# Kernel optimization log

Measured on AMD Instinct MI355X. Metric: run time of the kernel, lower is better.

The kernel has to match this reference:

```python
import jax, jax.numpy as jnp
import numpy as np
import math

B, C, H, W = 512, 64, 8, 8
E, NH, MEM = 64, 8, 8          # embed_dim, num_heads, mem_n
HD = E // NH                   # head_dim
THD = H * W * HD               # tot_head_dim = 512
AMB = 5.0                      # attn_mask_b
LN_EPS = 1e-5


def conv2d(x, w, b):
    y = jax.lax.conv_general_dilated(x, w, (1, 1), 'SAME',
                                     dimension_numbers=('NCHW', 'OIHW', 'NCHW'))
    return y + b[None, :, None, None]


def setup_inputs() -> dict:
    key = jax.random.key(0)
    ks = jax.random.split(key, 14)
    r = lambda k, s, sc=1.0: jax.random.normal(k, s, dtype=jnp.float32) * sc
    return {
        'input': r(ks[0], (B, C, H, W)),
        'h_cur': r(ks[1], (B, E, H, W)),
        'c_cur': r(ks[2], (B, E, H, W)),
        'concat_k': r(ks[3], (B, MEM, NH, THD)),
        'concat_v': r(ks[4], (B, MEM, NH, THD)),
        'attn_mask': jax.random.randint(ks[5], (B * NH, 1, MEM), 0, 2).astype(bool),
        'conv_w': r(ks[6], (5 * E, C + E, 3, 3), 0.05),
        'conv_b': jnp.zeros((5 * E,), jnp.float32),
        'proj_w': r(ks[7], (3 * E, C, 3, 3), 0.05),
        'proj_b': jnp.zeros((3 * E,), jnp.float32),
        'out_w': r(ks[8], (E, E, 3, 3), 0.05),
        'out_b': jnp.zeros((E,), jnp.float32),
        'ln_w': jnp.ones((E, H, W), jnp.float32),
        'ln_b': jnp.zeros((E, H, W), jnp.float32),
        'pos_w': r(ks[9], (MEM, H * W * E), 0.02),
        'pos_b': jax.random.uniform(ks[10], (MEM, NH), jnp.float32, -0.1, 0.1),
    }


def _cell(input, h_cur, c_cur, concat_k, concat_v, attn_mask,
          conv_w, conv_b, proj_w, proj_b, out_w, out_b, ln_w, ln_b, pos_w, pos_b):
    # ConvLSTM gates
    combined = jnp.concatenate([input, h_cur], axis=1)          # [B, C+E, H, W]
    cc = conv2d(combined, conv_w, conv_b)                       # [B, 5E, H, W]
    cc_i, cc_f, cc_o, cc_g, cc_a = jnp.split(cc, 5, axis=1)
    i = jax.nn.sigmoid(cc_i)
    f = jax.nn.sigmoid(cc_f)
    o = jax.nn.sigmoid(cc_o)
    g = jnp.tanh(cc_g)
    a = jax.nn.sigmoid(cc_a)
    c_next = f * c_cur + i * g

    # attention over growing memory
    kqv = conv2d(input, proj_w, proj_b)                         # [B, 3E, H, W]
    k, q, v = jnp.split(kqv, 3, axis=1)
    # [B, E, H, W] -> [B*NH, 1, THD] (contiguous split of E into NH heads)
    resh = lambda x: x.reshape(B * NH, 1, THD)
    k, q, v = resh(k), resh(q), resh(v)
    q_scaled = q / math.sqrt(THD)

    # prior memory: [B, MEM, NH, THD] -> [B*NH, MEM-1, THD]
    def mem_resh(m):
        return jnp.transpose(m[:, 1:], (1, 0, 2, 3)).reshape(MEM - 1, B * NH, THD).transpose(1, 0, 2)
    k_full = jnp.concatenate([mem_resh(concat_k), k], axis=1)   # [B*NH, MEM, THD]
    v_full = jnp.concatenate([mem_resh(concat_v), v], axis=1)

    # learned positional key offsets / score biases
    pos_w_e = jnp.broadcast_to(pos_w[:, None, :], (MEM, B, H * W * E)) \
                 .reshape(MEM, B * NH, THD).transpose(1, 0, 2)  # [B*NH, MEM, THD]
    pos_b_e = jnp.broadcast_to(pos_b[:, None, :], (MEM, B, NH)) \
                 .reshape(MEM, B * NH).T                        # [B*NH, MEM]
    k_full = k_full + pos_w_e

    # additive mask: -inf where masked, last slot forced to +attn_mask_b
    mask = jnp.where(attn_mask, -jnp.inf, 0.0).astype(q.dtype)  # [B*NH, 1, MEM]
    mask = mask.at[:, :, -1].set(AMB)

    scores = mask + jnp.einsum('bqd,bkd->bqk', q_scaled, k_full) + pos_b_e[:, None, :]
    w = jax.nn.softmax(scores, axis=-1)                         # [B*NH, 1, MEM]
    attn = jnp.einsum('bqk,bkd->bqd', w, v_full)                # [B*NH, 1, THD]
    attn = attn.reshape(B, E, H, W)

    out = conv2d(attn, out_w, out_b) + input[:, :E]
    # LayerNorm over (E, H, W)
    mu = jnp.mean(out, axis=(1, 2, 3), keepdims=True)
    var = jnp.mean((out - mu) ** 2, axis=(1, 2, 3), keepdims=True)
    out = (out - mu) / jnp.sqrt(var + LN_EPS) * ln_w[None] + ln_b[None]

    c_next = c_next + a * jnp.tanh(out)
    h_next = o * jnp.tanh(c_next)

    ret = lambda m: m.transpose(1, 0, 2).reshape(MEM, B, NH, THD).transpose(1, 0, 2, 3)
    return h_next, c_next, ret(k_full), ret(v_full)


def reference(input, h_cur, c_cur, concat_k, concat_v, attn_mask,
              conv_w, conv_b, proj_w, proj_b, out_w, out_b, ln_w, ln_b, pos_w, pos_b):
    return _cell(input, h_cur, c_cur, concat_k, concat_v, attn_mask,
                 conv_w, conv_b, proj_w, proj_b, out_w, out_b, ln_w, ln_b, pos_w, pos_b)
```

## Files before the change

kernel.cpp:

```cpp
#include <hip/hip_runtime.h>

typedef short short8 __attribute__((ext_vector_type(8)));
typedef __bf16 bf16x8 __attribute__((ext_vector_type(8)));
typedef float f32x4 __attribute__((ext_vector_type(4)));
typedef short s16x4 __attribute__((ext_vector_type(4)));
typedef unsigned u32x4 __attribute__((ext_vector_type(4)));

__device__ __forceinline__ short f2bf(float f) {
  unsigned u = __builtin_bit_cast(unsigned, f);
  u = (u + 0x7FFFu + ((u >> 16) & 1u)) >> 16;
  return (short)u;
}
__device__ __forceinline__ f32x4 mfma16(short8 a, short8 b, f32x4 c) {
  return __builtin_amdgcn_mfma_f32_16x16x32_bf16(
      __builtin_bit_cast(bf16x8, a), __builtin_bit_cast(bf16x8, b), c, 0, 0, 0);
}
__device__ __forceinline__ float sigm(float x) { return 1.0f / (1.0f + __expf(-x)); }
__device__ __forceinline__ float ftanh(float x) {
  return 1.0f - 2.0f / (1.0f + __expf(2.0f * x));
}
__device__ __forceinline__ f32x4 ld4(const float* p) { return *(const f32x4*)p; }
__device__ __forceinline__ void ntst4(float* p, f32x4 v) {
  __builtin_nontemporal_store(v, (f32x4*)p);
}

__global__ void pack_w(const float* __restrict__ w1, const float* __restrict__ w2,
                       const float* __restrict__ w3, short* __restrict__ out) {
  int e = blockIdx.x * 256 + threadIdx.x;
  if (e < 46080) {
    int kb8 = e / 320, n = e % 320;
    short8 v;
#pragma unroll
    for (int j = 0; j < 8; ++j) {
      int k = kb8 * 8 + j;
      int tap = k >> 7, ci = k & 127;
      v[j] = f2bf(w1[(n * 128 + ci) * 9 + tap]);
    }
    *(short8*)&out[e * 8] = v;
    return;
  }
  e -= 46080;
  if (e < 13824) {
    int kb8 = e / 192, n = e % 192;
    short8 v;
#pragma unroll
    for (int j = 0; j < 8; ++j) {
      int k = kb8 * 8 + j;
      int tap = k >> 6, ci = k & 63;
      v[j] = f2bf(w2[(n * 64 + ci) * 9 + tap]);
    }
    *(short8*)&out[(46080 + e) * 8] = v;
    return;
  }
  e -= 13824;
  {
    int kb8 = e / 64, n = e % 64;
    short8 v;
#pragma unroll
    for (int j = 0; j < 8; ++j) {
      int k = kb8 * 8 + j;
      int tap = k >> 6, ci = k & 63;
      v[j] = f2bf(w3[(n * 64 + ci) * 9 + tap]);
    }
    *(short8*)&out[(46080 + 13824 + e) * 8] = v;
  }
}

__launch_bounds__(512, 4)
__global__ void mid2_k(const float* __restrict__ input, const float* __restrict__ h_cur,
                       const float* __restrict__ c_cur, const float* __restrict__ ck,
                       const int* __restrict__ amask,
                       const float* __restrict__ conv_b, const float* __restrict__ proj_b,
                       const float* __restrict__ pos_w, const float* __restrict__ pos_b,
                       const short* __restrict__ pk1, const short* __restrict__ pk2,
                       float* __restrict__ o_k, float* __restrict__ o_v,
                       float* __restrict__ ws_wt, float* __restrict__ ws_ct,
                       unsigned* __restrict__ ws_oa) {
  __shared__ short comb[12800];
  __shared__ float Xb[4160];
  __shared__ float Vx[4160];
  __shared__ float sc_lds[8];
  float* combf = (float*)comb;
  unsigned* Xbu = (unsigned*)Xb;

  const int tid = threadIdx.x;
  const int wave = tid >> 6, lane = tid & 63;
  const int col = lane & 15, g4 = lane >> 4;
  const int wc = wave >> 1, wm = wave & 1;
  const int ch = wc * 16 + col;

  if (blockIdx.x < 512) {
    const int b = blockIdx.x;
    const int hd = wave;
    const int d0 = lane * 4, d1 = (lane + 64) * 4;
    if (tid < 8) sc_lds[tid] = 0.f;

#pragma unroll
    for (int i = 0; i < 2; ++i) {
      int idx = (tid + 512 * i) * 4;
      int c = idx >> 6, p0 = idx & 63;
      f32x4 vi = ld4(&input[b * 4096 + idx]);
#pragma unroll
      for (int j = 0; j < 4; ++j) {
        int p = p0 + j;
        int pp = ((p >> 3) + 1) * 10 + (p & 7) + 1;
        comb[pp * 64 + ((c + pp * 8) & 63)] = f2bf(vi[j]);
      }
    }
    for (int i = tid; i < 2304; i += 512) {
      int pr = i >> 6, c = i & 63;
      int pp = (pr < 10) ? pr
               : (pr < 20) ? (80 + pr)
               : (pr < 28) ? ((pr - 19) * 10)
                           : ((pr - 27) * 10 + 9);
      comb[pp * 64 + c] = 0;
    }
    __syncthreads();

    f32x4 acc2[2][3];
#pragma unroll
    for (int m = 0; m < 2; ++m)
#pragma unroll
      for (int g = 0; g < 3; ++g) acc2[m][g] = (f32x4){0.f, 0.f, 0.f, 0.f};
    short8 bb2[3];
#pragma unroll
    for (int g = 0; g < 3; ++g)
      bb2[g] = *(const short8*)&pk2[((g4)*192 + g * 64 + ch) * 8];
    for (int s = 0; s < 18; ++s) {
      short8 bbn[3];
      if (s < 17) {
        int kb8 = (s + 1) * 4 + g4;
#pragma unroll
        for (int g = 0; g < 3; ++g)
          bbn[g] = *(const short8*)&pk2[(kb8 * 192 + g * 64 + ch) * 8];
      }
      int tap = s >> 1, cib = s & 1;
      int kh = tap / 3, kw = tap % 3;
      short8 a[2];
#pragma unroll
      for (int m = 0; m < 2; ++m) {
        int p = (wm * 2 + m) * 16 + col;
        int pp = ((p >> 3) + kh) * 10 + (p & 7) + kw;
        int slot = (cib * 32 + g4 * 8 + pp * 8) & 63;
        a[m] = *(const short8*)&comb[pp * 64 + slot];
      }
#pragma unroll
      for (int m = 0; m < 2; ++m)
#pragma unroll
        for (int g = 0; g < 3; ++g) acc2[m][g] = mfma16(a[m], bb2[g], acc2[m][g]);
      if (s < 17) {
#pragma unroll
        for (int g = 0; g < 3; ++g) bb2[g] = bbn[g];
      }
    }

    float kreg[8], qreg[8], vreg[8], part7 = 0.f;
    {
      float pb0 = proj_b[ch], pb1 = proj_b[64 + ch], pb2 = proj_b[128 + ch];
      const float rsq = 0.044194173824159216f;
#pragma unroll
      for (int m = 0; m < 2; ++m)
#pragma unroll
        for (int r = 0; r < 4; ++r) {
          int p = (wm * 2 + m) * 16 + g4 * 4 + r;
          float kf = acc2[m][0][r] + pb0 + pos_w[7 * 4096 + ch * 64 + p];
          float qf = (acc2[m][1][r] + pb1) * rsq;
          float vf = acc2[m][2][r] + pb2;
          kreg[m * 4 + r] = kf;
          qreg[m * 4 + r] = qf;
          vreg[m * 4 + r] = vf;
          part7 = fmaf(qf, kf, part7);
        }
    }
    atomicAdd(&sc_lds[ch >> 3], part7);

    int msks[7];
    float pbv[7];
#pragma unroll
    for (int m = 0; m < 7; ++m) {
      msks[m] = amask[(b * 8 + hd) * 8 + m];
      pbv[m] = pos_b[m * 8 + hd];
    }

    __syncthreads();

#pragma unroll
    for (int m = 0; m < 2; ++m)
#pragma unroll
      for (int r = 0; r < 4; ++r) {
        int p = (wm * 2 + m) * 16 + g4 * 4 + r;
        combf[ch * 65 + p] = kreg[m * 4 + r];
        Xb[ch * 65 + p] = qreg[m * 4 + r];
        Vx[ch * 65 + p] = vreg[m * 4 + r];
      }
    __syncthreads();

    const size_t base7 = (size_t)(b * 64 + 56) * 512;
#pragma unroll
    for (int i = 0; i < 2; ++i) {
      int idx = (tid + 512 * i) * 4;
      int c = idx >> 6, p0 = idx & 63;
      f32x4 kq, vq;
#pragma unroll
      for (int j = 0; j < 4; ++j) {
        kq[j] = combf[c * 65 + p0 + j];
        vq[j] = Vx[c * 65 + p0 + j];
      }
      ntst4(&o_k[base7 + idx], kq);
      *(f32x4*)&o_v[base7 + idx] = vq;
    }
    const int cs0 = d0 >> 6, po0 = d0 & 63, cs1 = d1 >> 6, po1 = d1 & 63;
    f32x4 q0, q1;
#pragma unroll
    for (int j = 0; j < 4; ++j) {
      q0[j] = Xb[(hd * 8 + cs0) * 65 + po0 + j];
      q1[j] = Xb[(hd * 8 + cs1) * 65 + po1 + j];
    }
    float sc7 = sc_lds[hd] + pos_b[7 * 8 + hd] + 5.0f;

    float scv[8];
    scv[7] = sc7;
#pragma unroll
    for (int m = 0; m < 7; ++m) {
      const float* kp = ck + ((size_t)((b * 8 + m + 1) * 8 + hd)) * 512;
      const float* pw = pos_w + m * 4096 + hd * 512;
      f32x4 k0 = ld4(kp + d0) + ld4(pw + d0);
      f32x4 k1 = ld4(kp + d1) + ld4(pw + d1);
      float* dst = o_k + ((size_t)((b * 8 + m) * 8 + hd)) * 512;
      ntst4(dst + d0, k0);
      ntst4(dst + d1, k1);
      float part = 0.f;
#pragma unroll
      for (int j = 0; j < 4; ++j) {
        part = fmaf(q0[j], k0[j], part);
        part = fmaf(q1[j], k1[j], part);
      }
#pragma unroll
      for (int off = 32; off >= 1; off >>= 1) part += __shfl_xor(part, off);
      scv[m] = part + pbv[m] + (msks[m] ? -__builtin_inff() : 0.0f);
    }

    float mx = scv[0];
#pragma unroll
    for (int m = 1; m < 8; ++m) mx = fmaxf(mx, scv[m]);
    float w[8], s = 0.f;
#pragma unroll
    for (int m = 0; m < 8; ++m) {
      w[m] = __expf(scv[m] - mx);
      s += w[m];
    }
    float inv = 1.0f / s;
    if (lane == 0) {
#pragma unroll
      for (int m = 0; m < 8; ++m)
        ws_wt[(size_t)b * 64 + hd * 8 + m] = w[m] * inv;
    }
  } else {
    const int b = blockIdx.x - 512;
#pragma unroll
    for (int i = 0; i < 2; ++i) {
      int idx = (tid + 512 * i) * 4;
      int c = idx >> 6, p0 = idx & 63;
      f32x4 vi = ld4(&input[b * 4096 + idx]);
      f32x4 vh = ld4(&h_cur[b * 4096 + idx]);
      f32x4 vc = ld4(&c_cur[b * 4096 + idx]);
#pragma unroll
      for (int j = 0; j < 4; ++j) {
        int p = p0 + j;
        int pp = ((p >> 3) + 1) * 10 + (p & 7) + 1;
        comb[pp * 128 + ((c + pp * 8) & 127)] = f2bf(vi[j]);
        comb[pp * 128 + ((c + 64 + pp * 8) & 127)] = f2bf(vh[j]);
        Xb[c * 65 + p] = vc[j];
      }
    }
    for (int i = tid; i < 4608; i += 512) {
      int pr = i >> 7, c = i & 127;
      int pp = (pr < 10) ? pr
               : (pr < 20) ? (80 + pr)
               : (pr < 28) ? ((pr - 19) * 10)
                           : ((pr - 27) * 10 + 9);
      comb[pp * 128 + c] = 0;
    }
    __syncthreads();

    f32x4 acc1[2][5];
#pragma unroll
    for (int m = 0; m < 2; ++m)
#pragma unroll
      for (int g = 0; g < 5; ++g) acc1[m][g] = (f32x4){0.f, 0.f, 0.f, 0.f};
    short8 bb1[5];
#pragma unroll
    for (int g = 0; g < 5; ++g)
      bb1[g] = *(const short8*)&pk1[((g4)*320 + g * 64 + ch) * 8];
    for (int s = 0; s < 36; ++s) {
      short8 bbn[5];
      if (s < 35) {
        int kb8 = (s + 1) * 4 + g4;
#pragma unroll
        for (int g = 0; g < 5; ++g)
          bbn[g] = *(const short8*)&pk1[(kb8 * 320 + g * 64 + ch) * 8];
      }
      int tap = s >> 2, cib = s & 3;
      int kh = tap / 3, kw = tap % 3;
      short8 a[2];
#pragma unroll
      for (int m = 0; m < 2; ++m) {
        int p = (wm * 2 + m) * 16 + col;
        int pp = ((p >> 3) + kh) * 10 + (p & 7) + kw;
        int slot = (cib * 32 + g4 * 8 + pp * 8) & 127;
        a[m] = *(const short8*)&comb[pp * 128 + slot];
      }
#pragma unroll
      for (int m = 0; m < 2; ++m)
#pragma unroll
        for (int g = 0; g < 5; ++g) acc1[m][g] = mfma16(a[m], bb1[g], acc1[m][g]);
      if (s < 35) {
#pragma unroll
        for (int g = 0; g < 5; ++g) bb1[g] = bbn[g];
      }
    }

    float ctv[8];
    unsigned oav[8];
    {
      float bi0 = conv_b[ch], bi1 = conv_b[64 + ch], bi2 = conv_b[128 + ch];
      float bi3 = conv_b[192 + ch], bi4 = conv_b[256 + ch];
#pragma unroll
      for (int m = 0; m < 2; ++m)
#pragma unroll
        for (int r = 0; r < 4; ++r) {
          int p = (wm * 2 + m) * 16 + g4 * 4 + r;
          float iv = sigm(acc1[m][0][r] + bi0);
          float fv = sigm(acc1[m][1][r] + bi1);
          float ov = sigm(acc1[m][2][r] + bi2);
          float gv = ftanh(acc1[m][3][r] + bi3);
          float av = sigm(acc1[m][4][r] + bi4);
          ctv[m * 4 + r] = fv * Xb[ch * 65 + p] + iv * gv;
          oav[m * 4 + r] = ((unsigned)(unsigned short)f2bf(av) << 16) |
                           (unsigned)(unsigned short)f2bf(ov);
        }
    }
    __syncthreads();
#pragma unroll
    for (int m = 0; m < 2; ++m)
#pragma unroll
      for (int r = 0; r < 4; ++r) {
        int p = (wm * 2 + m) * 16 + g4 * 4 + r;
        combf[ch * 65 + p] = ctv[m * 4 + r];
        Xbu[ch * 65 + p] = oav[m * 4 + r];
      }
    __syncthreads();
#pragma unroll
    for (int i = 0; i < 2; ++i) {
      int idx = (tid + 512 * i) * 4;
      int c = idx >> 6, p0 = idx & 63;
      f32x4 cq;
      u32x4 oq;
#pragma unroll
      for (int j = 0; j < 4; ++j) {
        cq[j] = combf[c * 65 + p0 + j];
        oq[j] = Xbu[c * 65 + p0 + j];
      }
      *(f32x4*)&ws_ct[(size_t)b * 4096 + idx] = cq;
      *(u32x4*)&ws_oa[(size_t)b * 4096 + idx] = oq;
    }
  }
}

__launch_bounds__(512, 4)
__global__ void tail_k(const float* __restrict__ input, const float* __restrict__ cv,
                       const float* __restrict__ ws_wt,
                       const float* __restrict__ ws_ct,
                       const unsigned* __restrict__ ws_oa,
                       const float* __restrict__ out_b,
                       const float* __restrict__ ln_w, const float* __restrict__ ln_b,
                       const short* __restrict__ pk3,
                       float* __restrict__ o_h, float* __restrict__ o_c,
                       float* __restrict__ o_v) {
  __shared__ short comb[8320];
  __shared__ float Xb[4160];
  __shared__ float wt_s[64];
  __shared__ float red[16];
  float* combf = (float*)comb;
  unsigned* Xbu = (unsigned*)Xb;

  const int b = blockIdx.x;
  const int tid = threadIdx.x;
  const int wave = tid >> 6, lane = tid & 63;
  const int col = lane & 15, g4 = lane >> 4;
  const int wc = wave >> 1, wm = wave & 1;
  const int ch = wc * 16 + col;
  const int hd = wave;
  const int d0 = lane * 4, d1 = (lane + 64) * 4;

  f32x4 ctr[2];
  u32x4 oar[2];
#pragma unroll
  for (int i = 0; i < 2; ++i) {
    int idx = (tid + 512 * i) * 4;
    ctr[i] = ld4(&ws_ct[(size_t)b * 4096 + idx]);
    oar[i] = *(const u32x4*)&ws_oa[(size_t)b * 4096 + idx];
  }
  if (tid < 64) wt_s[tid] = ws_wt[(size_t)b * 64 + tid];

#pragma unroll
  for (int i = 0; i < 2; ++i) {
    int idx = (tid + 512 * i) * 4;
    int c = idx >> 6, p0 = idx & 63;
    f32x4 vi = ld4(&input[b * 4096 + idx]);
#pragma unroll
    for (int j = 0; j < 4; ++j) Xb[c * 65 + p0 + j] = vi[j];
  }
  for (int i = tid; i < 2304; i += 512) {
    int pr = i >> 6, c = i & 63;
    int pp = (pr < 10) ? pr
             : (pr < 20) ? (80 + pr)
             : (pr < 28) ? ((pr - 19) * 10)
                         : ((pr - 27) * 10 + 9);
    comb[pp * 64 + c] = 0;
  }
  __syncthreads();

  float wv[8];
#pragma unroll
  for (int m = 0; m < 8; ++m) wv[m] = wt_s[hd * 8 + m];

  f32x4 a0 = (f32x4){0.f, 0.f, 0.f, 0.f};
  f32x4 a1 = (f32x4){0.f, 0.f, 0.f, 0.f};
#pragma unroll
  for (int m = 0; m < 7; ++m) {
    const float* vp = cv + ((size_t)((b * 8 + m + 1) * 8 + hd)) * 512;
    f32x4 v0 = ld4(vp + d0);
    f32x4 v1 = ld4(vp + d1);
    float* dst = o_v + ((size_t)((b * 8 + m) * 8 + hd)) * 512;
    ntst4(dst + d0, v0);
    ntst4(dst + d1, v1);
    a0 += v0 * wv[m];
    a1 += v1 * wv[m];
  }
  {
    const float* vp = o_v + ((size_t)((b * 8 + 7) * 8 + hd)) * 512;
    a0 += ld4(vp + d0) * wv[7];
    a1 += ld4(vp + d1) * wv[7];
  }
#pragma unroll
  for (int j = 0; j < 4; ++j) {
    int dA = d0 + j, dB = d1 + j;
    int cA = hd * 8 + (dA >> 6), pA = dA & 63;
    int cB = hd * 8 + (dB >> 6), pB = dB & 63;
    int ppA = ((pA >> 3) + 1) * 10 + (pA & 7) + 1;
    int ppB = ((pB >> 3) + 1) * 10 + (pB & 7) + 1;
    comb[ppA * 64 + ((cA + ppA * 8) & 63)] = f2bf(a0[j]);
    comb[ppB * 64 + ((cB + ppB * 8) & 63)] = f2bf(a1[j]);
  }
  __syncthreads();

  f32x4 acc3[2];
  acc3[0] = (f32x4){0.f, 0.f, 0.f, 0.f};
  acc3[1] = (f32x4){0.f, 0.f, 0.f, 0.f};
  short8 bb3 = *(const short8*)&pk3[((g4)*64 + ch) * 8];
  for (int s = 0; s < 18; ++s) {
    short8 bbn;
    if (s < 17) {
      int kb8 = (s + 1) * 4 + g4;
      bbn = *(const short8*)&pk3[(kb8 * 64 + ch) * 8];
    }
    int tap = s >> 1, cib = s & 1;
    int kh = tap / 3, kw = tap % 3;
    short8 a[2];
#pragma unroll
    for (int m = 0; m < 2; ++m) {
      int p = (wm * 2 + m) * 16 + col;
      int pp = ((p >> 3) + kh) * 10 + (p & 7) + kw;
      int slot = (cib * 32 + g4 * 8 + pp * 8) & 63;
      a[m] = *(const short8*)&comb[pp * 64 + slot];
    }
#pragma unroll
    for (int m = 0; m < 2; ++m) acc3[m] = mfma16(a[m], bb3, acc3[m]);
    if (s < 17) bb3 = bbn;
  }

  float ov_[8], s1 = 0.f, s2 = 0.f;
  {
    float ob = out_b[ch];
#pragma unroll
    for (int m = 0; m < 2; ++m)
#pragma unroll
      for (int r = 0; r < 4; ++r) {
        int p = (wm * 2 + m) * 16 + g4 * 4 + r;
        float v = acc3[m][r] + ob + Xb[ch * 65 + p];
        ov_[m * 4 + r] = v;
        s1 += v;
        s2 += v * v;
      }
  }
#pragma unroll
  for (int off = 32; off >= 1; off >>= 1) {
    s1 += __shfl_xor(s1, off);
    s2 += __shfl_xor(s2, off);
  }
  if (lane == 0) { red[wave] = s1; red[8 + wave] = s2; }
  __syncthreads();
  float ts1 = 0.f, ts2 = 0.f;
#pragma unroll
  for (int w = 0; w < 8; ++w) { ts1 += red[w]; ts2 += red[8 + w]; }
  float mu = ts1 * (1.0f / 4096.0f);
  float var = ts2 * (1.0f / 4096.0f) - mu * mu;
  float rstd = rsqrtf(var + 1e-5f);

#pragma unroll
  for (int i = 0; i < 2; ++i) {
    int idx = (tid + 512 * i) * 4;
    int c = idx >> 6, p0 = idx & 63;
#pragma unroll
    for (int j = 0; j < 4; ++j) {
      combf[c * 65 + p0 + j] = ctr[i][j];
      Xbu[c * 65 + p0 + j] = oar[i][j];
    }
  }
  __syncthreads();

#pragma unroll
  for (int m = 0; m < 2; ++m)
#pragma unroll
    for (int r = 0; r < 4; ++r) {
      int p = (wm * 2 + m) * 16 + g4 * 4 + r;
      float ct = combf[ch * 65 + p];
      unsigned u = Xbu[ch * 65 + p];
      float og = __builtin_bit_cast(float, u << 16);
      float ag = __builtin_bit_cast(float, u & 0xffff0000u);
      float oln = (ov_[m * 4 + r] - mu) * rstd * ln_w[ch * 64 + p] + ln_b[ch * 64 + p];
      float cn = ct + ag * ftanh(oln);
      float hv = og * ftanh(cn);
      combf[ch * 65 + p] = hv;
      Xb[ch * 65 + p] = cn;
    }
  __syncthreads();
#pragma unroll
  for (int i = 0; i < 2; ++i) {
    int idx = (tid + 512 * i) * 4;
    int c = idx >> 6, p0 = idx & 63;
    f32x4 hq, cq;
#pragma unroll
    for (int j = 0; j < 4; ++j) {
      hq[j] = combf[c * 65 + p0 + j];
      cq[j] = Xb[c * 65 + p0 + j];
    }
    *(f32x4*)&o_h[b * 4096 + idx] = hq;
    *(f32x4*)&o_c[b * 4096 + idx] = cq;
  }
}

__launch_bounds__(512, 4)
__global__ void kqv_k(const float* __restrict__ input,
                      const float* __restrict__ proj_b,
                      const float* __restrict__ pos_w,
                      const short* __restrict__ pk2,
                      float* __restrict__ q_out, float* __restrict__ o_k,
                      float* __restrict__ o_v) {
  __shared__ short comb[6400];
  __shared__ float Xk[4160], Xq[4160], Xv[4160];
  const int b = blockIdx.x;
  const int tid = threadIdx.x;
  const int wave = tid >> 6, lane = tid & 63;
  const int col = lane & 15, g4 = lane >> 4;
  const int wc = wave >> 1, wm = wave & 1;
  const int ch = wc * 16 + col;
#pragma unroll
  for (int i = 0; i < 2; ++i) {
    int idx = (tid + 512 * i) * 4;
    int c = idx >> 6, p0 = idx & 63;
    f32x4 vi = ld4(&input[b * 4096 + idx]);
#pragma unroll
    for (int j = 0; j < 4; ++j) {
      int p = p0 + j;
      int pp = ((p >> 3) + 1) * 10 + (p & 7) + 1;
      comb[pp * 64 + ((c + pp * 8) & 63)] = f2bf(vi[j]);
    }
  }
  for (int i = tid; i < 2304; i += 512) {
    int pr = i >> 6, c = i & 63;
    int pp = (pr < 10) ? pr
             : (pr < 20) ? (80 + pr)
             : (pr < 28) ? ((pr - 19) * 10)
                         : ((pr - 27) * 10 + 9);
    comb[pp * 64 + c] = 0;
  }
  __syncthreads();
  f32x4 acc2[2][3];
#pragma unroll
  for (int m = 0; m < 2; ++m)
#pragma unroll
    for (int g = 0; g < 3; ++g) acc2[m][g] = (f32x4){0.f, 0.f, 0.f, 0.f};
  short8 bb2[3];
#pragma unroll
  for (int g = 0; g < 3; ++g)
    bb2[g] = *(const short8*)&pk2[((g4)*192 + g * 64 + ch) * 8];
  for (int s = 0; s < 18; ++s) {
    short8 bbn[3];
    if (s < 17) {
      int kb8 = (s + 1) * 4 + g4;
#pragma unroll
      for (int g = 0; g < 3; ++g)
        bbn[g] = *(const short8*)&pk2[(kb8 * 192 + g * 64 + ch) * 8];
    }
    int tap = s >> 1, cib = s & 1;
    int kh = tap / 3, kw = tap % 3;
    short8 a[2];
#pragma unroll
    for (int m = 0; m < 2; ++m) {
      int p = (wm * 2 + m) * 16 + col;
      int pp = ((p >> 3) + kh) * 10 + (p & 7) + kw;
      int slot = (cib * 32 + g4 * 8 + pp * 8) & 63;
      a[m] = *(const short8*)&comb[pp * 64 + slot];
    }
#pragma unroll
    for (int m = 0; m < 2; ++m)
#pragma unroll
      for (int g = 0; g < 3; ++g) acc2[m][g] = mfma16(a[m], bb2[g], acc2[m][g]);
    if (s < 17) {
#pragma unroll
      for (int g = 0; g < 3; ++g) bb2[g] = bbn[g];
    }
  }
  {
    float pb0 = proj_b[ch], pb1 = proj_b[64 + ch], pb2 = proj_b[128 + ch];
    const float rsq = 0.044194173824159216f;
#pragma unroll
    for (int m = 0; m < 2; ++m)
#pragma unroll
      for (int r = 0; r < 4; ++r) {
        int p = (wm * 2 + m) * 16 + g4 * 4 + r;
        Xk[ch * 65 + p] = acc2[m][0][r] + pb0 + pos_w[7 * 4096 + ch * 64 + p];
        Xq[ch * 65 + p] = (acc2[m][1][r] + pb1) * rsq;
        Xv[ch * 65 + p] = acc2[m][2][r] + pb2;
      }
  }
  __syncthreads();
  const size_t base7 = (size_t)(b * 64 + 56) * 512;
#pragma unroll
  for (int i = 0; i < 2; ++i) {
    int idx = (tid + 512 * i) * 4;
    int c = idx >> 6, p0 = idx & 63;
    f32x4 kq, qq, vq;
#pragma unroll
    for (int j = 0; j < 4; ++j) {
      kq[j] = Xk[c * 65 + p0 + j];
      qq[j] = Xq[c * 65 + p0 + j];
      vq[j] = Xv[c * 65 + p0 + j];
    }
    *(f32x4*)&o_k[base7 + idx] = kq;
    *(f32x4*)&q_out[(size_t)b * 4096 + idx] = qq;
    *(f32x4*)&o_v[base7 + idx] = vq;
  }
}

__launch_bounds__(64, 4)
__global__ void attn_k(const float* __restrict__ ck, const float* __restrict__ cv,
                       const int* __restrict__ amask,
                       const float* __restrict__ pos_w,
                       const float* __restrict__ pos_b,
                       const float* __restrict__ q_in,
                       float* __restrict__ o_k, float* __restrict__ o_v,
                       float* __restrict__ attn_out) {
  const int b = blockIdx.x >> 3;
  const int hd = blockIdx.x & 7;
  const int lane = threadIdx.x;
  const int d0 = lane * 4, d1 = (lane + 64) * 4;
  const float* qp = q_in + (size_t)b * 4096 + hd * 512;
  f32x4 q0 = ld4(qp + d0);
  f32x4 q1 = ld4(qp + d1);
  float sc[8];
#pragma unroll
  for (int m = 0; m < 7; ++m) {
    const float* kp = ck + ((size_t)((b * 8 + m + 1) * 8 + hd)) * 512;
    const float* pw = pos_w + m * 4096 + hd * 512;
    f32x4 k0 = ld4(kp + d0) + ld4(pw + d0);
    f32x4 k1 = ld4(kp + d1) + ld4(pw + d1);
    float* dst = o_k + ((size_t)((b * 8 + m) * 8 + hd)) * 512;
    ntst4(dst + d0, k0);
    ntst4(dst + d1, k1);
    float part = 0.f;
#pragma unroll
    for (int j = 0; j < 4; ++j) {
      part = fmaf(q0[j], k0[j], part);
      part = fmaf(q1[j], k1[j], part);
    }
#pragma unroll
    for (int off = 32; off >= 1; off >>= 1) part += __shfl_xor(part, off);
    float msk = amask[(b * 8 + hd) * 8 + m] ? -__builtin_inff() : 0.0f;
    sc[m] = part + pos_b[m * 8 + hd] + msk;
  }
  {
    const float* kp = o_k + ((size_t)((b * 8 + 7) * 8 + hd)) * 512;
    f32x4 k0 = ld4(kp + d0);
    f32x4 k1 = ld4(kp + d1);
    float part = 0.f;
#pragma unroll
    for (int j = 0; j < 4; ++j) {
      part = fmaf(q0[j], k0[j], part);
      part = fmaf(q1[j], k1[j], part);
    }
#pragma unroll
    for (int off = 32; off >= 1; off >>= 1) part += __shfl_xor(part, off);
    sc[7] = part + pos_b[7 * 8 + hd] + 5.0f;
  }
  float mx = sc[0];
#pragma unroll
  for (int m = 1; m < 8; ++m) mx = fmaxf(mx, sc[m]);
  float w[8], s = 0.f;
#pragma unroll
  for (int m = 0; m < 8; ++m) {
    w[m] = __expf(sc[m] - mx);
    s += w[m];
  }
  float inv = 1.0f / s;
#pragma unroll
  for (int m = 0; m < 8; ++m) w[m] *= inv;
  f32x4 a0 = (f32x4){0.f, 0.f, 0.f, 0.f};
  f32x4 a1 = (f32x4){0.f, 0.f, 0.f, 0.f};
#pragma unroll
  for (int m = 0; m < 7; ++m) {
    const float* vp = cv + ((size_t)((b * 8 + m + 1) * 8 + hd)) * 512;
    f32x4 v0 = ld4(vp + d0);
    f32x4 v1 = ld4(vp + d1);
    float* dst = o_v + ((size_t)((b * 8 + m) * 8 + hd)) * 512;
    ntst4(dst + d0, v0);
    ntst4(dst + d1, v1);
    a0 += v0 * w[m];
    a1 += v1 * w[m];
  }
  {
    const float* vp = o_v + ((size_t)((b * 8 + 7) * 8 + hd)) * 512;
    a0 += ld4(vp + d0) * w[7];
    a1 += ld4(vp + d1) * w[7];
  }
  float* ap = attn_out + (size_t)b * 4096 + hd * 512;
  *(f32x4*)&ap[d0] = a0;
  *(f32x4*)&ap[d1] = a1;
}

__launch_bounds__(512, 4)
__global__ void cell2_k(
    const float* __restrict__ input, const float* __restrict__ h_cur,
    const float* __restrict__ c_cur, const float* __restrict__ attn_in,
    const float* __restrict__ conv_b, const float* __restrict__ out_b,
    const float* __restrict__ ln_w, const float* __restrict__ ln_b,
    const short* __restrict__ pk1, const short* __restrict__ pk3,
    float* __restrict__ o_h, float* __restrict__ o_c) {
  __shared__ short comb[12800];
  __shared__ float Xb[4160];
  __shared__ float Qb[4160];
  __shared__ float Vb[4160];
  __shared__ float red[16];
  const int b = blockIdx.x;
  const int tid = threadIdx.x;
  const int wave = tid >> 6, lane = tid & 63;
  const int col = lane & 15, g4 = lane >> 4;
  const int wc = wave >> 1, wm = wave & 1;
  const int ch = wc * 16 + col;
#pragma unroll
  for (int i = 0; i < 2; ++i) {
    int idx = (tid + 512 * i) * 4;
    int c = idx >> 6, p0 = idx & 63;
    f32x4 vi = ld4(&input[b * 4096 + idx]);
    f32x4 vh = ld4(&h_cur[b * 4096 + idx]);
    f32x4 vc = ld4(&c_cur[b * 4096 + idx]);
#pragma unroll
    for (int j = 0; j < 4; ++j) {
      int p = p0 + j;
      int pp = ((p >> 3) + 1) * 10 + (p & 7) + 1;
      comb[pp * 128 + ((c + pp * 8) & 127)] = f2bf(vi[j]);
      comb[pp * 128 + ((c + 64 + pp * 8) & 127)] = f2bf(vh[j]);
      Xb[c * 65 + p] = vc[j];
    }
  }
  for (int i = tid; i < 4608; i += 512) {
    int pr = i >> 7, c = i & 127;
    int pp = (pr < 10) ? pr
             : (pr < 20) ? (80 + pr)
             : (pr < 28) ? ((pr - 19) * 10)
                         : ((pr - 27) * 10 + 9);
    comb[pp * 128 + c] = 0;
  }
  __syncthreads();
  f32x4 acc1[2][5];
#pragma unroll
  for (int m = 0; m < 2; ++m)
#pragma unroll
    for (int g = 0; g < 5; ++g) acc1[m][g] = (f32x4){0.f, 0.f, 0.f, 0.f};
  short8 bb1[5];
#pragma unroll
  for (int g = 0; g < 5; ++g)
    bb1[g] = *(const short8*)&pk1[((g4)*320 + g * 64 + ch) * 8];
  for (int s = 0; s < 36; ++s) {
    short8 bbn[5];
    if (s < 35) {
      int kb8 = (s + 1) * 4 + g4;
#pragma unroll
      for (int g = 0; g < 5; ++g)
        bbn[g] = *(const short8*)&pk1[(kb8 * 320 + g * 64 + ch) * 8];
    }
    int tap = s >> 2, cib = s & 3;
    int kh = tap / 3, kw = tap % 3;
    short8 a[2];
#pragma unroll
    for (int m = 0; m < 2; ++m) {
      int p = (wm * 2 + m) * 16 + col;
      int pp = ((p >> 3) + kh) * 10 + (p & 7) + kw;
      int slot = (cib * 32 + g4 * 8 + pp * 8) & 127;
      a[m] = *(const short8*)&comb[pp * 128 + slot];
    }
#pragma unroll
    for (int m = 0; m < 2; ++m)
#pragma unroll
      for (int g = 0; g < 5; ++g) acc1[m][g] = mfma16(a[m], bb1[g], acc1[m][g]);
    if (s < 35) {
#pragma unroll
      for (int g = 0; g < 5; ++g) bb1[g] = bbn[g];
    }
  }
  float ct_r[8], o_r[8], a_r[8];
  {
    float bi0 = conv_b[ch], bi1 = conv_b[64 + ch], bi2 = conv_b[128 + ch];
    float bi3 = conv_b[192 + ch], bi4 = conv_b[256 + ch];
#pragma unroll
    for (int m = 0; m < 2; ++m)
#pragma unroll
      for (int r = 0; r < 4; ++r) {
        int p = (wm * 2 + m) * 16 + g4 * 4 + r;
        float iv = sigm(acc1[m][0][r] + bi0);
        float fv = sigm(acc1[m][1][r] + bi1);
        float ov = sigm(acc1[m][2][r] + bi2);
        float gv = ftanh(acc1[m][3][r] + bi3);
        float av = sigm(acc1[m][4][r] + bi4);
        ct_r[m * 4 + r] = fv * Xb[ch * 65 + p] + iv * gv;
        o_r[m * 4 + r] = ov;
        a_r[m * 4 + r] = av;
      }
  }
  __syncthreads();
  {
    f32x4 av[2], iv[2];
#pragma unroll
    for (int i = 0; i < 2; ++i) {
      int idx = (tid + 512 * i) * 4;
      av[i] = ld4(&attn_in[b * 4096 + idx]);
      iv[i] = ld4(&input[b * 4096 + idx]);
    }
#pragma unroll
    for (int i = 0; i < 2; ++i) {
      int idx = (tid + 512 * i) * 4;
      int c = idx >> 6, p0 = idx & 63;
#pragma unroll
      for (int j = 0; j < 4; ++j) {
        int p = p0 + j;
        int pp = ((p >> 3) + 1) * 10 + (p & 7) + 1;
        comb[pp * 128 + ((c + pp * 8) & 127)] = f2bf(av[i][j]);
        Xb[c * 65 + p] = iv[i][j];
      }
    }
  }
  __syncthreads();
  f32x4 acc3[2];
  acc3[0] = (f32x4){0.f, 0.f, 0.f, 0.f};
  acc3[1] = (f32x4){0.f, 0.f, 0.f, 0.f};
  short8 bb3 = *(const short8*)&pk3[((g4)*64 + ch) * 8];
  for (int s = 0; s < 18; ++s) {
    short8 bbn;
    if (s < 17) {
      int kb8 = (s + 1) * 4 + g4;
      bbn = *(const short8*)&pk3[(kb8 * 64 + ch) * 8];
    }
    int tap = s >> 1, cib = s & 1;
    int kh = tap / 3, kw = tap % 3;
    short8 a[2];
#pragma unroll
    for (int m = 0; m < 2; ++m) {
      int p = (wm * 2 + m) * 16 + col;
      int pp = ((p >> 3) + kh) * 10 + (p & 7) + kw;
      int slot = (cib * 32 + g4 * 8 + pp * 8) & 127;
      a[m] = *(const short8*)&comb[pp * 128 + slot];
    }
#pragma unroll
    for (int m = 0; m < 2; ++m) acc3[m] = mfma16(a[m], bb3, acc3[m]);
    if (s < 17) bb3 = bbn;
  }
  float ov_[8], s1 = 0.f, s2 = 0.f;
  {
    float ob = out_b[ch];
#pragma unroll
    for (int m = 0; m < 2; ++m)
#pragma unroll
      for (int r = 0; r < 4; ++r) {
        int p = (wm * 2 + m) * 16 + g4 * 4 + r;
        float v = acc3[m][r] + ob + Xb[ch * 65 + p];
        ov_[m * 4 + r] = v;
        s1 += v;
        s2 += v * v;
      }
  }
#pragma unroll
  for (int off = 32; off >= 1; off >>= 1) {
    s1 += __shfl_xor(s1, off);
    s2 += __shfl_xor(s2, off);
  }
  if (lane == 0) { red[wave] = s1; red[8 + wave] = s2; }
  __syncthreads();
  float ts1 = 0.f, ts2 = 0.f;
#pragma unroll
  for (int w = 0; w < 8; ++w) { ts1 += red[w]; ts2 += red[8 + w]; }
  float mu = ts1 * (1.0f / 4096.0f);
  float var = ts2 * (1.0f / 4096.0f) - mu * mu;
  float rstd = rsqrtf(var + 1e-5f);
#pragma unroll
  for (int m = 0; m < 2; ++m)
#pragma unroll
    for (int r = 0; r < 4; ++r) {
      int p = (wm * 2 + m) * 16 + g4 * 4 + r;
      float oln = (ov_[m * 4 + r] - mu) * rstd * ln_w[ch * 64 + p] + ln_b[ch * 64 + p];
      float cn = ct_r[m * 4 + r] + a_r[m * 4 + r] * ftanh(oln);
      float hv = o_r[m * 4 + r] * ftanh(cn);
      Qb[ch * 65 + p] = hv;
      Vb[ch * 65 + p] = cn;
    }
  __syncthreads();
#pragma unroll
  for (int i = 0; i < 2; ++i) {
    int idx = (tid + 512 * i) * 4;
    int c = idx >> 6, p0 = idx & 63;
    f32x4 hv, cvv;
#pragma unroll
    for (int j = 0; j < 4; ++j) {
      hv[j] = Qb[c * 65 + p0 + j];
      cvv[j] = Vb[c * 65 + p0 + j];
    }
    *(f32x4*)&o_h[b * 4096 + idx] = hv;
    *(f32x4*)&o_c[b * 4096 + idx] = cvv;
  }
}

extern "C" void kernel_launch(void* const* d_in, const int* in_sizes, int n_in,
                              void* d_out, int out_size, void* d_ws, size_t ws_size,
                              hipStream_t stream) {
  (void)in_sizes; (void)n_in; (void)out_size;
  const float* input  = (const float*)d_in[0];
  const float* h_cur  = (const float*)d_in[1];
  const float* c_cur  = (const float*)d_in[2];
  const float* ck     = (const float*)d_in[3];
  const float* cv     = (const float*)d_in[4];
  const int*   amask  = (const int*)d_in[5];
  const float* conv_w = (const float*)d_in[6];
  const float* conv_b = (const float*)d_in[7];
  const float* proj_w = (const float*)d_in[8];
  const float* proj_b = (const float*)d_in[9];
  const float* out_w  = (const float*)d_in[10];
  const float* out_b  = (const float*)d_in[11];
  const float* ln_w   = (const float*)d_in[12];
  const float* ln_b   = (const float*)d_in[13];
  const float* pos_w  = (const float*)d_in[14];
  const float* pos_b  = (const float*)d_in[15];

  char* ws = (char*)d_ws;
  short* pk = (short*)ws;
  float* o_h = (float*)d_out;
  float* o_c = o_h + 2097152;
  float* o_k = o_h + 4194304;
  float* o_v = o_h + 20971520;

  pack_w<<<252, 256, 0, stream>>>(conv_w, proj_w, out_w, pk);

  if (ws_size >= (24u << 20)) {
    float* ws_wt = (float*)(ws + (2u << 20));
    float* ws_ct = (float*)(ws + (8u << 20));
    unsigned* ws_oa = (unsigned*)(ws + (16u << 20));
    mid2_k<<<1024, 512, 0, stream>>>(input, h_cur, c_cur, ck, amask,
                                     conv_b, proj_b, pos_w, pos_b,
                                     pk, pk + 368640,
                                     o_k, o_v, ws_wt, ws_ct, ws_oa);
    tail_k<<<512, 512, 0, stream>>>(input, cv, ws_wt, ws_ct, ws_oa,
                                    out_b, ln_w, ln_b, pk + 479232,
                                    o_h, o_c, o_v);
  } else {
    kqv_k<<<512, 512, 0, stream>>>(input, proj_b, pos_w, pk + 368640,
                                   o_h, o_k, o_v);
    attn_k<<<4096, 64, 0, stream>>>(ck, cv, amask, pos_w, pos_b, o_h,
                                    o_k, o_v, o_c);
    cell2_k<<<512, 512, 0, stream>>>(input, h_cur, c_cur, o_c,
                                     conv_b, out_b, ln_w, ln_b,
                                     pk, pk + 479232, o_h, o_c);
  }
}
```

Baseline: 99.34 us.

## Compute attention scores from MFMA register layout, dropping LDS transpose

```diff
diff --git a/kernel.cpp b/kernel.cpp
--- a/kernel.cpp
+++ b/kernel.cpp
@@ -67,7 +67,7 @@
 }
 
 __launch_bounds__(512, 4)
-__global__ void mid2_k(const float* __restrict__ input, const float* __restrict__ h_cur,
+__global__ void mid3_k(const float* __restrict__ input, const float* __restrict__ h_cur,
                        const float* __restrict__ c_cur, const float* __restrict__ ck,
                        const int* __restrict__ amask,
                        const float* __restrict__ conv_b, const float* __restrict__ proj_b,
@@ -78,8 +78,7 @@
                        unsigned* __restrict__ ws_oa) {
   __shared__ short comb[12800];
   __shared__ float Xb[4160];
-  __shared__ float Vx[4160];
-  __shared__ float sc_lds[8];
+  __shared__ float sc_part[128];
   float* combf = (float*)comb;
   unsigned* Xbu = (unsigned*)Xb;
 
@@ -91,9 +90,6 @@
 
   if (blockIdx.x < 512) {
     const int b = blockIdx.x;
-    const int hd = wave;
-    const int d0 = lane * 4, d1 = (lane + 64) * 4;
-    if (tid < 8) sc_lds[tid] = 0.f;
 
 #pragma unroll
     for (int i = 0; i < 2; ++i) {
@@ -154,106 +150,117 @@
       }
     }
 
-    float kreg[8], qreg[8], vreg[8], part7 = 0.f;
+    float kreg[8], qreg[8], vreg[8];
+    float part[8];
+#pragma unroll
+    for (int m = 0; m < 8; ++m) part[m] = 0.f;
     {
       float pb0 = proj_b[ch], pb1 = proj_b[64 + ch], pb2 = proj_b[128 + ch];
       const float rsq = 0.044194173824159216f;
 #pragma unroll
-      for (int m = 0; m < 2; ++m)
+      for (int m2 = 0; m2 < 2; ++m2) {
+        int p0 = wm * 32 + m2 * 16 + g4 * 4;
+        f32x4 pw7 = ld4(&pos_w[7 * 4096 + ch * 64 + p0]);
 #pragma unroll
         for (int r = 0; r < 4; ++r) {
-          int p = (wm * 2 + m) * 16 + g4 * 4 + r;
-          float kf = acc2[m][0][r] + pb0 + pos_w[7 * 4096 + ch * 64 + p];
-          float qf = (acc2[m][1][r] + pb1) * rsq;
-          float vf = acc2[m][2][r] + pb2;
-          kreg[m * 4 + r] = kf;
-          qreg[m * 4 + r] = qf;
-          vreg[m * 4 + r] = vf;
-          part7 = fmaf(qf, kf, part7);
+          float kf = acc2[m2][0][r] + pb0 + pw7[r];
+          float qf = (acc2[m2][1][r] + pb1) * rsq;
+          float vf = acc2[m2][2][r] + pb2;
+          kreg[m2 * 4 + r] = kf;
+          qreg[m2 * 4 + r] = qf;
+          vreg[m2 * 4 + r] = vf;
+          part[7] = fmaf(qf, kf, part[7]);
         }
-    }
-    atomicAdd(&sc_lds[ch >> 3], part7);
-
-    int msks[7];
-    float pbv[7];
+      }
+    }
+
+    const size_t base7 = (size_t)(b * 8 + 7) * 4096;
+#pragma unroll
+    for (int m2 = 0; m2 < 2; ++m2) {
+      int p0 = wm * 32 + m2 * 16 + g4 * 4;
+      f32x4 kq, vq;
+#pragma unroll
+      for (int r = 0; r < 4; ++r) {
+        kq[r] = kreg[m2 * 4 + r];
+        vq[r] = vreg[m2 * 4 + r];
+      }
+      *(f32x4*)&o_k[base7 + ch * 64 + p0] = kq;
+      *(f32x4*)&o_v[base7 + ch * 64 + p0] = vq;
+    }
+
 #pragma unroll
     for (int m = 0; m < 7; ++m) {
-      msks[m] = amask[(b * 8 + hd) * 8 + m];
-      pbv[m] = pos_b[m * 8 + hd];
-    }
-
+      const float* src = ck + (size_t)(b * 8 + m + 1) * 4096;
+      const float* pw = pos_w + m * 4096;
+      float* dst = o_k + (size_t)(b * 8 + m) * 4096;
+#pragma unroll
+      for (int i = 0; i < 2; ++i) {
+        int j = tid * 4 + i * 2048;
+        f32x4 k = ld4(src + j) + ld4(pw + j);
+        ntst4(dst + j, k);
+      }
+    }
+
+#pragma unroll
+    for (int m = 0; m < 7; ++m) {
+      const float* src = ck + (size_t)(b * 8 + m + 1) * 4096;
+      const float* pw = pos_w + m * 4096;
+#pragma unroll
+      for (int m2 = 0; m2 < 2; ++m2) {
+        int off = ch * 64 + wm * 32 + m2 * 16 + g4 * 4;
+        f32x4 kk = ld4(src + off) + ld4(pw + off);
+#pragma unroll
+        for (int r = 0; r < 4; ++r)
+          part[m] = fmaf(qreg[m2 * 4 + r], kk[r], part[m]);
+      }
+    }
+
+#pragma unroll
+    for (int m = 0; m < 8; ++m) {
+#pragma unroll
+      for (int msk = 0; msk < 5; ++msk) {
+        const int xm = (msk < 3) ? (1 << msk) : (2 << msk);
+        part[m] += __shfl_xor(part[m], xm);
+      }
+    }
+    if (lane < 16) {
+      float myv = part[0];
+#pragma unroll
+      for (int m = 1; m < 8; ++m)
+        if ((lane & 7) == m) myv = part[m];
+      sc_part[wave * 16 + lane] = myv;
+    }
     __syncthreads();
 
-#pragma unroll
-    for (int m = 0; m < 2; ++m)
-#pragma unroll
-      for (int r = 0; r < 4; ++r) {
-        int p = (wm * 2 + m) * 16 + g4 * 4 + r;
-        combf[ch * 65 + p] = kreg[m * 4 + r];
-        Xb[ch * 65 + p] = qreg[m * 4 + r];
-        Vx[ch * 65 + p] = vreg[m * 4 + r];
-      }
-    __syncthreads();
-
-    const size_t base7 = (size_t)(b * 64 + 56) * 512;
-#pragma unroll
-    for (int i = 0; i < 2; ++i) {
-      int idx = (tid + 512 * i) * 4;
-      int c = idx >> 6, p0 = idx & 63;
-      f32x4 kq, vq;
-#pragma unroll
-      for (int j = 0; j < 4; ++j) {
-        kq[j] = combf[c * 65 + p0 + j];
-        vq[j] = Vx[c * 65 + p0 + j];
-      }
-      ntst4(&o_k[base7 + idx], kq);
-      *(f32x4*)&o_v[base7 + idx] = vq;
-    }
-    const int cs0 = d0 >> 6, po0 = d0 & 63, cs1 = d1 >> 6, po1 = d1 & 63;
-    f32x4 q0, q1;
-#pragma unroll
-    for (int j = 0; j < 4; ++j) {
-      q0[j] = Xb[(hd * 8 + cs0) * 65 + po0 + j];
-      q1[j] = Xb[(hd * 8 + cs1) * 65 + po1 + j];
-    }
-    float sc7 = sc_lds[hd] + pos_b[7 * 8 + hd] + 5.0f;
-
-    float scv[8];
-    scv[7] = sc7;
-#pragma unroll
-    for (int m = 0; m < 7; ++m) {
-      const float* kp = ck + ((size_t)((b * 8 + m + 1) * 8 + hd)) * 512;
-      const float* pw = pos_w + m * 4096 + hd * 512;
-      f32x4 k0 = ld4(kp + d0) + ld4(pw + d0);
-      f32x4 k1 = ld4(kp + d1) + ld4(pw + d1);
-      float* dst = o_k + ((size_t)((b * 8 + m) * 8 + hd)) * 512;
-      ntst4(dst + d0, k0);
-      ntst4(dst + d1, k1);
-      float part = 0.f;
-#pragma unroll
-      for (int j = 0; j < 4; ++j) {
-        part = fmaf(q0[j], k0[j], part);
-        part = fmaf(q1[j], k1[j], part);
-      }
-#pragma unroll
-      for (int off = 32; off >= 1; off >>= 1) part += __shfl_xor(part, off);
-      scv[m] = part + pbv[m] + (msks[m] ? -__builtin_inff() : 0.0f);
-    }
-
-    float mx = scv[0];
-#pragma unroll
-    for (int m = 1; m < 8; ++m) mx = fmaxf(mx, scv[m]);
-    float w[8], s = 0.f;
-#pragma unroll
-    for (int m = 0; m < 8; ++m) {
-      w[m] = __expf(scv[m] - mx);
-      s += w[m];
-    }
-    float inv = 1.0f / s;
-    if (lane == 0) {
+    if (tid < 8) {
+      const int head = tid;
+      const int w0 = (head >> 1) * 2, hbit = head & 1;
+      float scv[8];
+#pragma unroll
+      for (int m = 0; m < 8; ++m) {
+        float tot = sc_part[w0 * 16 + hbit * 8 + m] +
+                    sc_part[(w0 + 1) * 16 + hbit * 8 + m];
+        float extra;
+        if (m < 7)
+          extra = pos_b[m * 8 + head] +
+                  (amask[(b * 8 + head) * 8 + m] ? -__builtin_inff() : 0.0f);
+        else
+          extra = pos_b[56 + head] + 5.0f;
+        scv[m] = tot + extra;
+      }
+      float mx = scv[0];
+#pragma unroll
+      for (int m = 1; m < 8; ++m) mx = fmaxf(mx, scv[m]);
+      float w[8], s = 0.f;
+#pragma unroll
+      for (int m = 0; m < 8; ++m) {
+        w[m] = __expf(scv[m] - mx);
+        s += w[m];
+      }
+      float inv = 1.0f / s;
 #pragma unroll
       for (int m = 0; m < 8; ++m)
-        ws_wt[(size_t)b * 64 + hd * 8 + m] = w[m] * inv;
+        ws_wt[(size_t)b * 64 + head * 8 + m] = w[m] * inv;
     }
   } else {
     const int b = blockIdx.x - 512;
@@ -974,7 +981,7 @@
     float* ws_wt = (float*)(ws + (2u << 20));
     float* ws_ct = (float*)(ws + (8u << 20));
     unsigned* ws_oa = (unsigned*)(ws + (16u << 20));
-    mid2_k<<<1024, 512, 0, stream>>>(input, h_cur, c_cur, ck, amask,
+    mid3_k<<<1024, 512, 0, stream>>>(input, h_cur, c_cur, ck, amask,
                                      conv_b, proj_b, pos_w, pos_b,
                                      pk, pk + 368640,
                                      o_k, o_v, ws_wt, ws_ct, ws_oa);
```

Measured after the change: 104.8 us. 5.5% more time.
